# Performance work log

Measured on AMD Instinct MI355X. Metric: run time of the kernel, lower is better.

The kernel has to match this reference:

```python
import jax, jax.numpy as jnp
import numpy as np

EPS = 1e-5

def rmsnorm(x, g):
    var = jnp.mean(jnp.square(x), axis=-1, keepdims=True)
    return x * jax.lax.rsqrt(var + EPS) * g

def setup_inputs() -> dict:
    key = jax.random.key(0)
    ks = jax.random.split(key, 8)
    B, S, T, D = 2, 2048, 2048, 1024
    H, HKV, HD = 16, 4, 64
    std = 0.02
    return {
        "x": jax.random.normal(ks[0], (B, S, D), jnp.float32),
        "kv": jax.random.normal(ks[1], (B, T, D), jnp.float32),
        "wq": jax.random.normal(ks[2], (H * HD, D), jnp.float32) * std,
        "wk": jax.random.normal(ks[3], (HKV * HD, D), jnp.float32) * std,
        "wv": jax.random.normal(ks[4], (HKV * HD, D), jnp.float32) * std,
        "wo": jax.random.normal(ks[5], (D, H * HD), jnp.float32) * std,
        "gq": jnp.ones((D,), jnp.float32),
        "gkv": jnp.ones((D,), jnp.float32),
    }

def reference(x, kv, wq, wk, wv, wo, gq, gkv):
    B, S, D = x.shape
    T = kv.shape[1]
    H, HKV, HD = 16, 4, 64
    R = H // HKV  # heads per kv group
    xn = rmsnorm(x, gq)
    kvn = rmsnorm(kv, gkv)
    # projections
    q = (xn @ wq.T).reshape(B, S, HKV, R, HD)   # grouped query heads
    k = (kvn @ wk.T).reshape(B, T, HKV, HD)
    v = (kvn @ wv.T).reshape(B, T, HKV, HD)
    scale = 1.0 / jnp.sqrt(jnp.float32(HD))
    # block-mask is None -> full dense cross attention; GQA via broadcast einsum
    scores = jnp.einsum('bsgrd,btgd->bgrst', q, k) * scale  # [B,HKV,R,S,T]
    probs = jax.nn.softmax(scores, axis=-1)
    out = jnp.einsum('bgrst,btgd->bsgrd', probs, v)  # [B,S,HKV,R,HD]
    out = out.reshape(B, S, H * HD) @ wo.T
    return x + out
```

## Files before the change

### kernel.cpp

```cpp
#include <hip/hip_runtime.h>

#define DEV __device__ __forceinline__

typedef __attribute__((ext_vector_type(8))) _Float16 h8;
typedef __attribute__((ext_vector_type(4))) float f32x4;
typedef __attribute__((ext_vector_type(16))) float f32x16;
typedef __fp16 __attribute__((ext_vector_type(2))) hh2;

DEV unsigned short f2h(float f) {
  union { _Float16 h[2]; unsigned short u[2]; } v;
  v.h[0] = (_Float16)f;
  return v.u[0];
}

DEV float h2f(unsigned short u) {
  union { _Float16 h[2]; unsigned short u[2]; } v;
  v.u[0] = u;
  return (float)v.h[0];
}

DEV void async_load16(const void* g, void* l) {
  __builtin_amdgcn_global_load_lds(
      (const __attribute__((address_space(1))) void*)g,
      (__attribute__((address_space(3))) void*)l,
      16, 0, 0);
}

DEV void pl32swap(unsigned int& a, unsigned int& b) {
  asm("v_permlane32_swap_b32 %0, %1" : "+v"(a), "+v"(b));
}


__global__ __launch_bounds__(256) void prep(const float* __restrict__ x,
                                            const float* __restrict__ kv,
                                            const float* __restrict__ wq,
                                            const float* __restrict__ wk,
                                            const float* __restrict__ wv,
                                            const float* __restrict__ wo,
                                            const float* __restrict__ gq,
                                            const float* __restrict__ gkv,
                                            unsigned short* __restrict__ wqb,
                                            unsigned short* __restrict__ wkvb,
                                            unsigned short* __restrict__ wob,
                                            unsigned short* __restrict__ xn,
                                            unsigned short* __restrict__ kvn,
                                            float qscale) {
  const int b = blockIdx.x, tid = threadIdx.x;
  if (b < 2560) {
    const float* src;
    unsigned short* dst;
    float sc = 1.0f;
    int base;
    if (b < 1024) { src = wq; dst = wqb; sc = qscale; base = b; }
    else if (b < 1280) { src = wk; dst = wkvb; base = b - 1024; }
    else if (b < 1536) { src = wv; dst = wkvb + 262144; base = b - 1280; }
    else { src = wo; dst = wob; base = b - 1536; }
    const int i = (base * 256 + tid) * 4;
    float4 v = *(const float4*)&src[i];
    ushort4 o;
    o.x = f2h(v.x * sc); o.y = f2h(v.y * sc);
    o.z = f2h(v.z * sc); o.w = f2h(v.w * sc);
    *(ushort4*)&dst[i] = o;
    return;
  }
  int row = b - 2560;
  const float* src;
  const float* g;
  unsigned short* dst;
  if (row < 4096) { src = x; g = gq; dst = xn; }
  else { row -= 4096; src = kv; g = gkv; dst = kvn; }
  const float* xr = src + (size_t)row * 1024;
  float4 v = *(const float4*)&xr[tid * 4];
  float ss = v.x * v.x + v.y * v.y + v.z * v.z + v.w * v.w;
  ss += __shfl_xor(ss, 32); ss += __shfl_xor(ss, 16);
  ss += __shfl_xor(ss, 8);  ss += __shfl_xor(ss, 4);
  ss += __shfl_xor(ss, 2);  ss += __shfl_xor(ss, 1);
  __shared__ float red[4];
  if ((tid & 63) == 0) red[tid >> 6] = ss;
  __syncthreads();
  float tot = red[0] + red[1] + red[2] + red[3];
  float inv = rsqrtf(tot * (1.0f / 1024.0f) + 1e-5f);
  float4 gv = *(const float4*)&g[tid * 4];
  ushort4 o;
  o.x = f2h(v.x * inv * gv.x); o.y = f2h(v.y * inv * gv.y);
  o.z = f2h(v.z * inv * gv.z); o.w = f2h(v.w * inv * gv.w);
  *(ushort4*)&dst[(size_t)row * 1024 + tid * 4] = o;
}

__global__ __launch_bounds__(256) void proj_gemm(const unsigned short* __restrict__ xn,
                                                 const unsigned short* __restrict__ kvn,
                                                 const unsigned short* __restrict__ wqb,
                                                 const unsigned short* __restrict__ wkvb,
                                                 unsigned short* __restrict__ qb,
                                                 unsigned short* __restrict__ kb,
                                                 unsigned short* __restrict__ vTb) {
  __shared__ unsigned short Al[2][2][128 * 32];
  __shared__ unsigned short Bl[2][2][64 * 32];
  const int tid = threadIdx.x;
  const int w = tid >> 6, l = tid & 63;
  const int quad = l >> 4, ln = l & 15;
  const int wm0 = (w >> 1) * 64, wn0 = (w & 1) * 32;
  const int r4 = l >> 2;
  const int c4s = (((l & 3) ^ ((l >> 3) & 3))) * 8;
  const int qs8 = (quad ^ ((l >> 1) & 3)) * 8;

  int z = blockIdx.x;
  const unsigned short *A, *W;
  int m0, n0, isq;
  if (z < 512) {
    A = xn; W = wqb; isq = 1;
    m0 = (((z >> 7) << 3) + (z & 7)) * 128;
    n0 = ((z >> 3) & 15) * 64;
  } else {
    z -= 512; A = kvn; W = wkvb; isq = 0;
    m0 = (((z >> 6) << 3) + (z & 7)) * 128;
    n0 = ((z >> 3) & 7) * 64;
  }

  f32x4 acc[4][2] = {};

  auto stage = [&](int buf, int kk) {
#pragma unroll
    for (int j = 0; j < 6; ++j) {
      const int idx = w * 6 + j;
      if (idx < 16) {
        const int p = idx >> 3, rb = (idx & 7) * 16;
        async_load16(A + (size_t)(m0 + rb + r4) * 1024 + kk + p * 32 + c4s,
                     &Al[buf][p][rb * 32]);
      } else {
        const int ib = idx - 16;
        const int p = ib >> 2, rb = (ib & 3) * 16;
        async_load16(W + (size_t)(n0 + rb + r4) * 1024 + kk + p * 32 + c4s,
                     &Bl[buf][p][rb * 32]);
      }
    }
  };

  stage(0, 0);
#pragma unroll 2
  for (int it = 0; it < 16; ++it) {
    const int buf = it & 1;
    __syncthreads();
    if (it < 15) stage(buf ^ 1, (it + 1) * 64);
#pragma unroll
    for (int kc = 0; kc < 2; ++kc) {
      h8 af[4], bf[2];
#pragma unroll
      for (int mi = 0; mi < 4; ++mi)
        af[mi] = *(const h8*)&Al[buf][kc][(wm0 + mi * 16 + ln) * 32 + qs8];
#pragma unroll
      for (int ni = 0; ni < 2; ++ni)
        bf[ni] = *(const h8*)&Bl[buf][kc][(wn0 + ni * 16 + ln) * 32 + qs8];
#pragma unroll
      for (int mi = 0; mi < 4; ++mi)
#pragma unroll
        for (int ni = 0; ni < 2; ++ni)
          acc[mi][ni] = __builtin_amdgcn_mfma_f32_16x16x32_f16(af[mi], bf[ni], acc[mi][ni], 0, 0, 0);
    }
  }

#pragma unroll
  for (int mi = 0; mi < 4; ++mi)
#pragma unroll
    for (int ni = 0; ni < 2; ++ni)
#pragma unroll
      for (int r = 0; r < 4; ++r) {
        const int row = m0 + wm0 + mi * 16 + quad * 4 + r;
        const int col = n0 + wn0 + ni * 16 + ln;
        const unsigned short v = f2h(acc[mi][ni][r]);
        if (isq) {
          qb[((size_t)row << 10) + col] = v;
        } else if (col < 256) {
          kb[(size_t)row * 256 + col] = v;
        } else {
          const int c2 = col - 256, gg = c2 >> 6, dd = c2 & 63;
          const int bb = row >> 11, t = row & 2047;
          vTb[((size_t)((bb * 4 + gg) * 64 + dd) << 11) + t] = v;
        }
      }
}

__global__ __launch_bounds__(256) void o_gemm(const unsigned short* __restrict__ O0,
                                              const unsigned short* __restrict__ O1,
                                              const float* __restrict__ l0p,
                                              const float* __restrict__ l1p,
                                              const unsigned short* __restrict__ wob,
                                              const float* __restrict__ x,
                                              float* __restrict__ out) {
  __shared__ unsigned short Al[2][2][128 * 32];
  __shared__ unsigned short Bl[2][2][64 * 32];
  __shared__ float Linv[16 * 128];
  const int tid = threadIdx.x;
  const int w = tid >> 6, l = tid & 63;
  const int quad = l >> 4, ln = l & 15;
  const int wm0 = (w >> 1) * 64, wn0 = (w & 1) * 32;
  const int r4 = l >> 2;
  const int c4s = (((l & 3) ^ ((l >> 3) & 3))) * 8;
  const int qs8 = (quad ^ ((l >> 1) & 3)) * 8;

  const int z = blockIdx.x;
  const int m0 = (((z >> 7) << 3) + (z & 7)) * 128;
  const int n0 = ((z >> 3) & 15) * 64;

  {
    const int h = tid >> 4, r0 = (tid & 15) * 8;
#pragma unroll
    for (int i = 0; i < 8; ++i) {
      const int r = r0 + i;
      const size_t li = (size_t)(m0 + r) * 16 + h;
      Linv[h * 128 + r] = 1.0f / (l0p[li] + l1p[li]);
    }
  }
  __syncthreads();

  const int srow = tid >> 3;
  const int sp = (tid >> 2) & 1;
  const int ss = tid & 3;

  auto stageA = [&](int buf, int kk) {
    const int h = kk >> 6;
#pragma unroll
    for (int ps = 0; ps < 4; ++ps) {
      const int row = ps * 32 + srow;
      const size_t gidx = (size_t)(m0 + row) * 1024 + kk + sp * 32 + ss * 8;
      h8 a0 = *(const h8*)&O0[gidx];
      h8 a1 = *(const h8*)&O1[gidx];
      const _Float16 lv = (_Float16)Linv[h * 128 + row];
      h8 sum = a0 + a1;
#pragma unroll
      for (int q2 = 0; q2 < 8; ++q2) sum[q2] *= lv;
      const int sl = ss ^ ((row >> 1) & 3);
      *(h8*)&Al[buf][sp][row * 32 + sl * 8] = sum;
    }
  };
  auto stageB = [&](int buf, int kk) {
#pragma unroll
    for (int j = 0; j < 2; ++j) {
      const int ib = w * 2 + j;
      const int p = ib >> 2, rb = (ib & 3) * 16;
      async_load16(wob + (size_t)(n0 + rb + r4) * 1024 + kk + p * 32 + c4s,
                   &Bl[buf][p][rb * 32]);
    }
  };

  f32x4 acc[4][2] = {};
  stageB(0, 0);
  stageA(0, 0);
  for (int it = 0; it < 16; ++it) {
    const int buf = it & 1;
    __syncthreads();
    if (it < 15) { stageB(buf ^ 1, (it + 1) * 64); stageA(buf ^ 1, (it + 1) * 64); }
#pragma unroll
    for (int kc = 0; kc < 2; ++kc) {
      h8 af[4], bf[2];
#pragma unroll
      for (int mi = 0; mi < 4; ++mi)
        af[mi] = *(const h8*)&Al[buf][kc][(wm0 + mi * 16 + ln) * 32 + qs8];
#pragma unroll
      for (int ni = 0; ni < 2; ++ni)
        bf[ni] = *(const h8*)&Bl[buf][kc][(wn0 + ni * 16 + ln) * 32 + qs8];
#pragma unroll
      for (int mi = 0; mi < 4; ++mi)
#pragma unroll
        for (int ni = 0; ni < 2; ++ni)
          acc[mi][ni] = __builtin_amdgcn_mfma_f32_16x16x32_f16(af[mi], bf[ni], acc[mi][ni], 0, 0, 0);
    }
  }

#pragma unroll
  for (int mi = 0; mi < 4; ++mi)
#pragma unroll
    for (int ni = 0; ni < 2; ++ni)
#pragma unroll
      for (int r = 0; r < 4; ++r) {
        const int row = m0 + wm0 + mi * 16 + quad * 4 + r;
        const int col = n0 + wn0 + ni * 16 + ln;
        const size_t idx = ((size_t)row << 10) + col;
        out[idx] = x[idx] + acc[mi][ni][r];
      }
}

__global__ __launch_bounds__(256, 3) void flash_attn(const unsigned short* __restrict__ q,
                                                     const unsigned short* __restrict__ k,
                                                     const unsigned short* __restrict__ vT,
                                                     unsigned short* __restrict__ o0,
                                                     unsigned short* __restrict__ o1,
                                                     float* __restrict__ l0p,
                                                     float* __restrict__ l1p) {
  __shared__ __align__(16) unsigned short Kl[3][64 * 64];
  __shared__ __align__(16) unsigned short Vl[3][64 * 64];

  const int tid = threadIdx.x;
  const int w = tid >> 6, l = tid & 63;
  const int lq = l & 31, hi = l >> 5;
  const int r8 = l >> 3, c8 = l & 7;
  const int csw = (c8 ^ r8) * 8;
  const int rsw = lq & 7;
  const int s0 = blockIdx.x * 128;
  const int h = blockIdx.y, g = h >> 2;
  const int b = blockIdx.z >> 1, ts = blockIdx.z & 1;
  const int tbase = ts << 10;

  unsigned short* Opart = ts ? o1 : o0;
  float* lpart = ts ? l1p : l0p;

  const size_t qrow = (size_t)(b * 2048 + s0 + w * 32 + lq);

  h8 qf[4];
#pragma unroll
  for (int ks = 0; ks < 4; ++ks)
    qf[ks] = *(const h8*)&q[(qrow << 10) + h * 64 + ks * 16 + hi * 8];
  asm volatile("s_waitcnt vmcnt(0)" ::: "memory");

  int aoff[4];
#pragma unroll
  for (int j = 0; j < 4; ++j)
    aoff[j] = (lq * 64 + (((2 * j + hi) ^ rsw)) * 8) * 2;

  f32x16 oacc[2] = {};
  float lsA = 0.0f, lsB = 0.0f;

  const unsigned short* kbase = k + ((size_t)(b * 2048)) * 256 + g * 64;
  const unsigned short* vbase = vT + (((size_t)(b * 4 + g) * 64) << 11);

  const hh2 one2 = {(__fp16)1.0f, (__fp16)1.0f};

  auto stage = [&](int sb, int t0) {
#pragma unroll
    for (int j = 0; j < 2; ++j) {
      const int idx = w * 2 + j;
      async_load16(kbase + (size_t)(t0 + idx * 8 + r8) * 256 + csw,
                   &Kl[sb][idx * 512]);
      async_load16(vbase + (((size_t)(idx * 8 + r8)) << 11) + t0 + csw,
                   &Vl[sb][idx * 512]);
    }
  };

#define FA_SYNC(N)                                                   \
  do {                                                               \
    asm volatile("s_waitcnt vmcnt(" #N ")" ::: "memory");            \
    __builtin_amdgcn_s_barrier();                                    \
    __builtin_amdgcn_sched_barrier(0);                               \
  } while (0)

#define FA_BODY(CB)                                                            \
  {                                                                            \
    h8 kf0[4], kf1[4];                                                         \
    _Pragma("unroll")                                                          \
    for (int ks = 0; ks < 4; ++ks) {                                           \
      kf0[ks] = *(const h8*)((const char*)&Kl[CB][0] + aoff[ks]);              \
      kf1[ks] = *(const h8*)((const char*)&Kl[CB][2048] + aoff[ks]);           \
    }                                                                          \
    f32x16 st0 = {}, st1 = {};                                                 \
    __builtin_amdgcn_s_setprio(1);                                             \
    _Pragma("unroll")                                                          \
    for (int ks = 0; ks < 4; ++ks) {                                           \
      st0 = __builtin_amdgcn_mfma_f32_32x32x16_f16(kf0[ks], qf[ks], st0, 0, 0, 0); \
      st1 = __builtin_amdgcn_mfma_f32_32x32x16_f16(kf1[ks], qf[ks], st1, 0, 0, 0); \
    }                                                                          \
    __builtin_amdgcn_s_setprio(0);                                             \
    unsigned int w0_[8], w1_[8];                                               \
    _Pragma("unroll")                                                          \
    for (int j = 0; j < 8; ++j) {                                              \
      union { hh2 h2; unsigned int u; } pk0, pk1;                              \
      pk0.h2 = __builtin_amdgcn_cvt_pkrtz(__builtin_amdgcn_exp2f(st0[2 * j]),  \
                                          __builtin_amdgcn_exp2f(st0[2 * j + 1])); \
      pk1.h2 = __builtin_amdgcn_cvt_pkrtz(__builtin_amdgcn_exp2f(st1[2 * j]),  \
                                          __builtin_amdgcn_exp2f(st1[2 * j + 1])); \
      lsA = __builtin_amdgcn_fdot2(pk0.h2, one2, lsA, false);                  \
      lsB = __builtin_amdgcn_fdot2(pk1.h2, one2, lsB, false);                  \
      w0_[j] = pk0.u; w1_[j] = pk1.u;                                          \
    }                                                                          \
    h8 pf[4];                                                                  \
    {                                                                          \
      unsigned int a0 = w0_[0], b0 = w0_[2]; pl32swap(a0, b0);                 \
      unsigned int a1 = w0_[1], b1 = w0_[3]; pl32swap(a1, b1);                 \
      unsigned int a4 = w0_[4], b4 = w0_[6]; pl32swap(a4, b4);                 \
      unsigned int a5 = w0_[5], b5 = w0_[7]; pl32swap(a5, b5);                 \
      union { unsigned int u[4]; h8 v; } f0, f1;                               \
      f0.u[0] = a0; f0.u[1] = a1; f0.u[2] = b0; f0.u[3] = b1;                  \
      f1.u[0] = a4; f1.u[1] = a5; f1.u[2] = b4; f1.u[3] = b5;                  \
      pf[0] = f0.v; pf[1] = f1.v;                                              \
      unsigned int c0 = w1_[0], d0 = w1_[2]; pl32swap(c0, d0);                 \
      unsigned int c1 = w1_[1], d1 = w1_[3]; pl32swap(c1, d1);                 \
      unsigned int c4 = w1_[4], d4 = w1_[6]; pl32swap(c4, d4);                 \
      unsigned int c5 = w1_[5], d5 = w1_[7]; pl32swap(c5, d5);                 \
      union { unsigned int u[4]; h8 v; } f2, f3;                               \
      f2.u[0] = c0; f2.u[1] = c1; f2.u[2] = d0; f2.u[3] = d1;                  \
      f3.u[0] = c4; f3.u[1] = c5; f3.u[2] = d4; f3.u[3] = d5;                  \
      pf[2] = f2.v; pf[3] = f3.v;                                              \
    }                                                                          \
    __builtin_amdgcn_s_setprio(1);                                             \
    _Pragma("unroll")                                                          \
    for (int c = 0; c < 4; ++c) {                                              \
      h8 v0 = *(const h8*)((const char*)&Vl[CB][0] + aoff[c]);                 \
      h8 v1 = *(const h8*)((const char*)&Vl[CB][2048] + aoff[c]);              \
      oacc[0] = __builtin_amdgcn_mfma_f32_32x32x16_f16(v0, pf[c], oacc[0], 0, 0, 0); \
      oacc[1] = __builtin_amdgcn_mfma_f32_32x32x16_f16(v1, pf[c], oacc[1], 0, 0, 0); \
    }                                                                          \
    __builtin_amdgcn_s_setprio(0);                                             \
  }

  stage(0, tbase);
  stage(1, tbase + 64);

  for (int tt = 0; tt < 15; tt += 3) {
    FA_SYNC(4);
    stage(2, tbase + (tt + 2) * 64);
    FA_BODY(0);
    FA_SYNC(4);
    stage(0, tbase + (tt + 3) * 64);
    FA_BODY(1);
    FA_SYNC(4);
    if (tt + 4 < 16) stage(1, tbase + (tt + 4) * 64);
    FA_BODY(2);
  }
  FA_SYNC(0);
  FA_BODY(0);

#undef FA_BODY
#undef FA_SYNC

  float lsum = lsA + lsB;
  lsum += __shfl_xor(lsum, 32);
  if (l < 32) lpart[qrow * 16 + h] = lsum;

#pragma unroll
  for (int dblk = 0; dblk < 2; ++dblk)
#pragma unroll
    for (int qd = 0; qd < 4; ++qd) {
      ushort4 o;
      o.x = f2h(oacc[dblk][qd * 4 + 0]);
      o.y = f2h(oacc[dblk][qd * 4 + 1]);
      o.z = f2h(oacc[dblk][qd * 4 + 2]);
      o.w = f2h(oacc[dblk][qd * 4 + 3]);
      *(ushort4*)&Opart[(qrow << 10) + h * 64 + dblk * 32 + qd * 8 + hi * 4] = o;
    }
}

extern "C" void kernel_launch(void* const* d_in, const int* in_sizes, int n_in,
                              void* d_out, int out_size, void* d_ws, size_t ws_size,
                              hipStream_t stream) {
  const float* x   = (const float*)d_in[0];
  const float* kv  = (const float*)d_in[1];
  const float* wq  = (const float*)d_in[2];
  const float* wk  = (const float*)d_in[3];
  const float* wv  = (const float*)d_in[4];
  const float* wo  = (const float*)d_in[5];
  const float* gq  = (const float*)d_in[6];
  const float* gkv = (const float*)d_in[7];

  char* ws = (char*)d_ws;
  unsigned short* xn   = (unsigned short*)(ws);
  unsigned short* kvn  = (unsigned short*)(ws + 8388608);
  unsigned short* qb   = (unsigned short*)(ws + 16777216);
  unsigned short* kb   = (unsigned short*)(ws + 25165824);
  unsigned short* vTb  = (unsigned short*)(ws + 27262976);
  unsigned short* wqb  = (unsigned short*)(ws + 37748736);
  unsigned short* wkvb = (unsigned short*)(ws + 39845888);
  unsigned short* wob  = (unsigned short*)(ws + 40894464);
  unsigned short* Opart0 = xn;
  unsigned short* Opart1 = kvn;
  float* l0p = (float*)wqb;
  float* l1p = (float*)(ws + 37748736 + 262144);

  const float qscale = 0.18033688011112042f;

  prep<<<10752, 256, 0, stream>>>(x, kv, wq, wk, wv, wo, gq, gkv,
                                  wqb, wkvb, wob, xn, kvn, qscale);

  proj_gemm<<<768, 256, 0, stream>>>(xn, kvn, wqb, wkvb, qb, kb, vTb);

  flash_attn<<<dim3(16, 16, 4), 256, 0, stream>>>(qb, kb, vTb, Opart0, Opart1, l0p, l1p);

  o_gemm<<<512, 256, 0, stream>>>(Opart0, Opart1, l0p, l1p, wob, x, (float*)d_out);
}
```

Before: 194.4 us.

## Process 64 query rows per wave in flash attention to reuse K/V fragments

Each wave now handles two 32-row query tiles (256 rows per block), so every K and V fragment read from shared memory feeds two MFMAs instead of one. The key block is split into two halves so register pressure stays manageable. The grid halves in x and the launch bound drops to 2 blocks per CU. The aim is to cut LDS traffic and staging per unit of work, at the cost of more registers, fewer blocks (512 instead of 1024) and lower occupancy.

```diff
diff --git a/kernel.cpp b/kernel.cpp
--- a/kernel.cpp
+++ b/kernel.cpp
@@ -280,7 +280,7 @@
       }
 }
 
-__global__ __launch_bounds__(256, 3) void flash_attn(const unsigned short* __restrict__ q,
+__global__ __launch_bounds__(256, 2) void flash_attn(const unsigned short* __restrict__ q,
                                                      const unsigned short* __restrict__ k,
                                                      const unsigned short* __restrict__ vT,
                                                      unsigned short* __restrict__ o0,
@@ -296,7 +296,7 @@
   const int r8 = l >> 3, c8 = l & 7;
   const int csw = (c8 ^ r8) * 8;
   const int rsw = lq & 7;
-  const int s0 = blockIdx.x * 128;
+  const int s0 = blockIdx.x * 256;
   const int h = blockIdx.y, g = h >> 2;
   const int b = blockIdx.z >> 1, ts = blockIdx.z & 1;
   const int tbase = ts << 10;
@@ -304,12 +304,16 @@
   unsigned short* Opart = ts ? o1 : o0;
   float* lpart = ts ? l1p : l0p;
 
-  const size_t qrow = (size_t)(b * 2048 + s0 + w * 32 + lq);
-
-  h8 qf[4];
-#pragma unroll
-  for (int ks = 0; ks < 4; ++ks)
-    qf[ks] = *(const h8*)&q[(qrow << 10) + h * 64 + ks * 16 + hi * 8];
+  size_t qrow[2];
+  qrow[0] = (size_t)(b * 2048 + s0 + w * 64 + lq);
+  qrow[1] = qrow[0] + 32;
+
+  h8 qf[2][4];
+#pragma unroll
+  for (int q2 = 0; q2 < 2; ++q2)
+#pragma unroll
+    for (int ks = 0; ks < 4; ++ks)
+      qf[q2][ks] = *(const h8*)&q[(qrow[q2] << 10) + h * 64 + ks * 16 + hi * 8];
   asm volatile("s_waitcnt vmcnt(0)" ::: "memory");
 
   int aoff[4];
@@ -317,8 +321,8 @@
   for (int j = 0; j < 4; ++j)
     aoff[j] = (lq * 64 + (((2 * j + hi) ^ rsw)) * 8) * 2;
 
-  f32x16 oacc[2] = {};
-  float lsA = 0.0f, lsB = 0.0f;
+  f32x16 oacc[2][2] = {};
+  float lsum[2] = {0.0f, 0.0f};
 
   const unsigned short* kbase = k + ((size_t)(b * 2048)) * 256 + g * 64;
   const unsigned short* vbase = vT + (((size_t)(b * 4 + g) * 64) << 11);
@@ -343,20 +347,18 @@
     __builtin_amdgcn_sched_barrier(0);                               \
   } while (0)
 
-#define FA_BODY(CB)                                                            \
+#define FA_HALF(CB, TH)                                                        \
   {                                                                            \
-    h8 kf0[4], kf1[4];                                                         \
+    h8 kf[4];                                                                  \
     _Pragma("unroll")                                                          \
-    for (int ks = 0; ks < 4; ++ks) {                                           \
-      kf0[ks] = *(const h8*)((const char*)&Kl[CB][0] + aoff[ks]);              \
-      kf1[ks] = *(const h8*)((const char*)&Kl[CB][2048] + aoff[ks]);           \
-    }                                                                          \
+    for (int ks = 0; ks < 4; ++ks)                                             \
+      kf[ks] = *(const h8*)((const char*)&Kl[CB][(TH) * 2048] + aoff[ks]);     \
     f32x16 st0 = {}, st1 = {};                                                 \
     __builtin_amdgcn_s_setprio(1);                                             \
     _Pragma("unroll")                                                          \
     for (int ks = 0; ks < 4; ++ks) {                                           \
-      st0 = __builtin_amdgcn_mfma_f32_32x32x16_f16(kf0[ks], qf[ks], st0, 0, 0, 0); \
-      st1 = __builtin_amdgcn_mfma_f32_32x32x16_f16(kf1[ks], qf[ks], st1, 0, 0, 0); \
+      st0 = __builtin_amdgcn_mfma_f32_32x32x16_f16(kf[ks], qf[0][ks], st0, 0, 0, 0); \
+      st1 = __builtin_amdgcn_mfma_f32_32x32x16_f16(kf[ks], qf[1][ks], st1, 0, 0, 0); \
     }                                                                          \
     __builtin_amdgcn_s_setprio(0);                                             \
     unsigned int w0_[8], w1_[8];                                               \
@@ -367,11 +369,11 @@
                                           __builtin_amdgcn_exp2f(st0[2 * j + 1])); \
       pk1.h2 = __builtin_amdgcn_cvt_pkrtz(__builtin_amdgcn_exp2f(st1[2 * j]),  \
                                           __builtin_amdgcn_exp2f(st1[2 * j + 1])); \
-      lsA = __builtin_amdgcn_fdot2(pk0.h2, one2, lsA, false);                  \
-      lsB = __builtin_amdgcn_fdot2(pk1.h2, one2, lsB, false);                  \
+      lsum[0] = __builtin_amdgcn_fdot2(pk0.h2, one2, lsum[0], false);          \
+      lsum[1] = __builtin_amdgcn_fdot2(pk1.h2, one2, lsum[1], false);          \
       w0_[j] = pk0.u; w1_[j] = pk1.u;                                          \
     }                                                                          \
-    h8 pf[4];                                                                  \
+    h8 pf0[2], pf1[2];                                                         \
     {                                                                          \
       unsigned int a0 = w0_[0], b0 = w0_[2]; pl32swap(a0, b0);                 \
       unsigned int a1 = w0_[1], b1 = w0_[3]; pl32swap(a1, b1);                 \
@@ -380,7 +382,7 @@
       union { unsigned int u[4]; h8 v; } f0, f1;                               \
       f0.u[0] = a0; f0.u[1] = a1; f0.u[2] = b0; f0.u[3] = b1;                  \
       f1.u[0] = a4; f1.u[1] = a5; f1.u[2] = b4; f1.u[3] = b5;                  \
-      pf[0] = f0.v; pf[1] = f1.v;                                              \
+      pf0[0] = f0.v; pf0[1] = f1.v;                                            \
       unsigned int c0 = w1_[0], d0 = w1_[2]; pl32swap(c0, d0);                 \
       unsigned int c1 = w1_[1], d1 = w1_[3]; pl32swap(c1, d1);                 \
       unsigned int c4 = w1_[4], d4 = w1_[6]; pl32swap(c4, d4);                 \
@@ -388,18 +390,23 @@
       union { unsigned int u[4]; h8 v; } f2, f3;                               \
       f2.u[0] = c0; f2.u[1] = c1; f2.u[2] = d0; f2.u[3] = d1;                  \
       f3.u[0] = c4; f3.u[1] = c5; f3.u[2] = d4; f3.u[3] = d5;                  \
-      pf[2] = f2.v; pf[3] = f3.v;                                              \
+      pf1[0] = f2.v; pf1[1] = f3.v;                                            \
     }                                                                          \
     __builtin_amdgcn_s_setprio(1);                                             \
     _Pragma("unroll")                                                          \
-    for (int c = 0; c < 4; ++c) {                                              \
+    for (int cc = 0; cc < 2; ++cc) {                                           \
+      const int c = (TH) * 2 + cc;                                             \
       h8 v0 = *(const h8*)((const char*)&Vl[CB][0] + aoff[c]);                 \
       h8 v1 = *(const h8*)((const char*)&Vl[CB][2048] + aoff[c]);              \
-      oacc[0] = __builtin_amdgcn_mfma_f32_32x32x16_f16(v0, pf[c], oacc[0], 0, 0, 0); \
-      oacc[1] = __builtin_amdgcn_mfma_f32_32x32x16_f16(v1, pf[c], oacc[1], 0, 0, 0); \
+      oacc[0][0] = __builtin_amdgcn_mfma_f32_32x32x16_f16(v0, pf0[cc], oacc[0][0], 0, 0, 0); \
+      oacc[1][0] = __builtin_amdgcn_mfma_f32_32x32x16_f16(v0, pf1[cc], oacc[1][0], 0, 0, 0); \
+      oacc[0][1] = __builtin_amdgcn_mfma_f32_32x32x16_f16(v1, pf0[cc], oacc[0][1], 0, 0, 0); \
+      oacc[1][1] = __builtin_amdgcn_mfma_f32_32x32x16_f16(v1, pf1[cc], oacc[1][1], 0, 0, 0); \
     }                                                                          \
     __builtin_amdgcn_s_setprio(0);                                             \
   }
+
+#define FA_BODY(CB) { FA_HALF(CB, 0) FA_HALF(CB, 1) }
 
   stage(0, tbase);
   stage(1, tbase + 64);
@@ -419,23 +426,26 @@
   FA_BODY(0);
 
 #undef FA_BODY
+#undef FA_HALF
 #undef FA_SYNC
 
-  float lsum = lsA + lsB;
-  lsum += __shfl_xor(lsum, 32);
-  if (l < 32) lpart[qrow * 16 + h] = lsum;
-
-#pragma unroll
-  for (int dblk = 0; dblk < 2; ++dblk)
-#pragma unroll
-    for (int qd = 0; qd < 4; ++qd) {
-      ushort4 o;
-      o.x = f2h(oacc[dblk][qd * 4 + 0]);
-      o.y = f2h(oacc[dblk][qd * 4 + 1]);
-      o.z = f2h(oacc[dblk][qd * 4 + 2]);
-      o.w = f2h(oacc[dblk][qd * 4 + 3]);
-      *(ushort4*)&Opart[(qrow << 10) + h * 64 + dblk * 32 + qd * 8 + hi * 4] = o;
-    }
+#pragma unroll
+  for (int q2 = 0; q2 < 2; ++q2) {
+    float ls = lsum[q2];
+    ls += __shfl_xor(ls, 32);
+    if (l < 32) lpart[qrow[q2] * 16 + h] = ls;
+#pragma unroll
+    for (int dblk = 0; dblk < 2; ++dblk)
+#pragma unroll
+      for (int qd = 0; qd < 4; ++qd) {
+        ushort4 o;
+        o.x = f2h(oacc[q2][dblk][qd * 4 + 0]);
+        o.y = f2h(oacc[q2][dblk][qd * 4 + 1]);
+        o.z = f2h(oacc[q2][dblk][qd * 4 + 2]);
+        o.w = f2h(oacc[q2][dblk][qd * 4 + 3]);
+        *(ushort4*)&Opart[(qrow[q2] << 10) + h * 64 + dblk * 32 + qd * 8 + hi * 4] = o;
+      }
+  }
 }
 
 extern "C" void kernel_launch(void* const* d_in, const int* in_sizes, int n_in,
@@ -471,7 +481,7 @@
 
   proj_gemm<<<768, 256, 0, stream>>>(xn, kvn, wqb, wkvb, qb, kb, vTb);
 
-  flash_attn<<<dim3(16, 16, 4), 256, 0, stream>>>(qb, kb, vTb, Opart0, Opart1, l0p, l1p);
+  flash_attn<<<dim3(8, 16, 4), 256, 0, stream>>>(qb, kb, vTb, Opart0, Opart1, l0p, l1p);
 
   o_gemm<<<512, 256, 0, stream>>>(Opart0, Opart1, l0p, l1p, wob, x, (float*)d_out);
 }
```

Result: faster. 190.4 us (-2.1%).
